# Kernel optimization log

Hardware: AMD Instinct MI355X
Metric: run time of the kernel (lower is better)

## Reference

```python
import jax, jax.numpy as jnp
import numpy as np

NUM_HEADS = 16
NUM_KV_HEADS = 8
HEAD_DIM = 256
HIDDEN = 2048
ROT_DIM = 64          # head_dim * partial_rotary_factor (0.25)
RMS_EPS = 1e-6
ROPE_THETA = 10000.0
SEQ = 2048


def _rmsnorm(x, weight=None):
    # Gemma RMSNorm: x * rsqrt(mean(x^2)+eps) * (1 + w); v_norm has no scale.
    var = jnp.mean(jnp.square(x), axis=-1, keepdims=True)
    n = x * jax.lax.rsqrt(var + RMS_EPS)
    if weight is not None:
        n = n * (1.0 + weight)
    return n


def _rope(x, positions):
    # Partial neox-style RoPE on the first ROT_DIM dims of each head.
    # x: [S, H, D]
    rot, rest = x[..., :ROT_DIM], x[..., ROT_DIM:]
    half = ROT_DIM // 2
    inv_freq = 1.0 / (ROPE_THETA ** (jnp.arange(0, ROT_DIM, 2, dtype=jnp.float32) / ROT_DIM))
    freqs = positions.astype(jnp.float32)[:, None] * inv_freq  # [S, half]
    cos = jnp.cos(freqs)[:, None, :]  # [S, 1, half]
    sin = jnp.sin(freqs)[:, None, :]
    x1, x2 = rot[..., :half], rot[..., half:]
    rot_out = jnp.concatenate([x1 * cos - x2 * sin, x2 * cos + x1 * sin], axis=-1)
    return jnp.concatenate([rot_out, rest], axis=-1)


def setup_inputs() -> dict:
    key = jax.random.key(0)
    k1, k2, k3, k4, k5 = jax.random.split(key, 5)
    q_size = NUM_HEADS * HEAD_DIM
    kv_size = NUM_KV_HEADS * HEAD_DIM
    return {
        "positions": jnp.arange(SEQ, dtype=jnp.int32),
        "hidden_states": jax.random.normal(k1, (SEQ, HIDDEN), dtype=jnp.float32),
        "w_qkv": jax.random.normal(k2, (q_size + 2 * kv_size, HIDDEN), dtype=jnp.float32) * (HIDDEN ** -0.5),
        "q_norm_w": jax.random.normal(k3, (HEAD_DIM,), dtype=jnp.float32) * 0.02,
        "k_norm_w": jax.random.normal(k4, (HEAD_DIM,), dtype=jnp.float32) * 0.02,
        "w_o": jax.random.normal(k5, (HIDDEN, q_size), dtype=jnp.float32) * (q_size ** -0.5),
    }


def reference(positions, hidden_states, w_qkv, q_norm_w, k_norm_w, w_o):
    S = hidden_states.shape[0]
    q_size = NUM_HEADS * HEAD_DIM
    kv_size = NUM_KV_HEADS * HEAD_DIM

    qkv = hidden_states @ w_qkv.T  # [S, q+2kv]
    q, k, v = jnp.split(qkv, [q_size, q_size + kv_size], axis=-1)
    q = q.reshape(S, NUM_HEADS, HEAD_DIM)
    k = k.reshape(S, NUM_KV_HEADS, HEAD_DIM)
    v = v.reshape(S, NUM_KV_HEADS, HEAD_DIM)

    # per-head RMSNorms (v_norm: scale_shift=0, with_scale=False -> pure norm)
    q = _rmsnorm(q, q_norm_w)
    k = _rmsnorm(k, k_norm_w)
    v = _rmsnorm(v, None)

    q = _rope(q, positions)
    k = _rope(k, positions)

    # GQA: repeat kv heads to match query heads
    rep = NUM_HEADS // NUM_KV_HEADS
    k = jnp.repeat(k, rep, axis=1)  # [S, H, D]
    v = jnp.repeat(v, rep, axis=1)

    # RadixAttention constructed with scaling=1.0 -> no 1/sqrt(d) scale
    scores = jnp.einsum("qhd,khd->hqk", q, k)  # [H, S, S]
    causal = positions[:, None] >= positions[None, :]  # [S, S]
    scores = jnp.where(causal[None, :, :], scores, jnp.float32(-1e30))
    attn = jax.nn.softmax(scores, axis=-1)
    out = jnp.einsum("hqk,khd->qhd", attn, v)  # [S, H, D]
    out = out.reshape(S, q_size)
    return out @ w_o.T  # [S, HIDDEN]
```

## Files before the change

### kernel.cpp

```cpp
#include <hip/hip_runtime.h>
#include <stdint.h>
#include <math.h>

#define SEQ 2048
#define HID 2048
#define NH 16
#define NKV 8
#define HD 256
#define QSZ 4096
#define QKVN 8192

typedef __attribute__((ext_vector_type(4))) float f32x4;
typedef _Float16 f16x8 __attribute__((ext_vector_type(8)));
typedef unsigned short u16;

__device__ __forceinline__ u16 f2h(float f) {
  _Float16 h = (_Float16)f;
  return __builtin_bit_cast(u16, h);
}
__device__ __forceinline__ float h2f(u16 b) {
  return (float)__builtin_bit_cast(_Float16, b);
}
__device__ __forceinline__ void glds16(const void* g, void* l) {
  __builtin_amdgcn_global_load_lds(
      (const __attribute__((address_space(1))) uint32_t*)g,
      (__attribute__((address_space(3))) uint32_t*)l, 16, 0, 0);
}

__global__ void cvt_f32_f16(const float* __restrict__ in, u16* __restrict__ out, int n4) {
  int i = blockIdx.x * 256 + threadIdx.x;
  if (i < n4) {
    float4 v = reinterpret_cast<const float4*>(in)[i];
    ushort4 o = make_ushort4(f2h(v.x), f2h(v.y), f2h(v.z), f2h(v.w));
    reinterpret_cast<ushort4*>(out)[i] = o;
  }
}

template <int F16OUT>
__global__ __launch_bounds__(256, 2) void gemm_bt(
    const u16* __restrict__ A, const u16* __restrict__ B, void* __restrict__ Cv,
    int M, int N, int K) {
  __shared__ __align__(16) u16 As[128 * 32];
  __shared__ __align__(16) u16 Bs[128 * 32];
  const int t = threadIdx.x;
  const int w = t >> 6, l = t & 63;
  const int bm = blockIdx.y * 128, bn = blockIdx.x * 128;
  const int wr = (w >> 1) * 64, wc = (w & 1) * 64;
  f32x4 acc[4][4] = {};

  const int arow = t >> 2;
  const int acol = (t & 3) * 8;
  const u16* Ag0 = A + (size_t)(bm + arow) * K + acol;
  const u16* Ag1 = A + (size_t)(bm + 64 + arow) * K + acol;
  const u16* Bg0 = B + (size_t)(bn + arow) * K + acol;
  const u16* Bg1 = B + (size_t)(bn + 64 + arow) * K + acol;
  u16* Al0 = As + w * 512;
  u16* Al1 = As + 2048 + w * 512;
  u16* Bl0 = Bs + w * 512;
  u16* Bl1 = Bs + 2048 + w * 512;

  const int lr = l & 15;
  const int lko = (l >> 4) * 8;

  for (int k0 = 0; k0 < K; k0 += 32) {
    __syncthreads();
    glds16(Ag0 + k0, Al0);
    glds16(Ag1 + k0, Al1);
    glds16(Bg0 + k0, Bl0);
    glds16(Bg1 + k0, Bl1);
    __syncthreads();
    f16x8 a[4], b[4];
#pragma unroll
    for (int m = 0; m < 4; ++m) a[m] = *(const f16x8*)&As[(wr + m * 16 + lr) * 32 + lko];
#pragma unroll
    for (int n = 0; n < 4; ++n) b[n] = *(const f16x8*)&Bs[(wc + n * 16 + lr) * 32 + lko];
#pragma unroll
    for (int m = 0; m < 4; ++m)
#pragma unroll
      for (int n = 0; n < 4; ++n)
        acc[m][n] = __builtin_amdgcn_mfma_f32_16x16x32_f16(a[m], b[n], acc[m][n], 0, 0, 0);
  }

#pragma unroll
  for (int m = 0; m < 4; ++m) {
#pragma unroll
    for (int n = 0; n < 4; ++n) {
      const int col = bn + wc + n * 16 + lr;
      const int row0 = bm + wr + m * 16 + (l >> 4) * 4;
#pragma unroll
      for (int j = 0; j < 4; ++j) {
        float vv = acc[m][n][j];
        if constexpr (F16OUT)
          ((u16*)Cv)[(size_t)(row0 + j) * N + col] = f2h(vv);
        else
          ((float*)Cv)[(size_t)(row0 + j) * N + col] = vv;
      }
    }
  }
}

__global__ void norm_rope(const u16* __restrict__ qkv, const float* __restrict__ qw,
                          const float* __restrict__ kw, const int* __restrict__ pos,
                          u16* __restrict__ qo, u16* __restrict__ ko, u16* __restrict__ vt) {
  const int b = blockIdx.x;
  const int s = b >> 5;
  const int slot = b & 31;
  const int l = threadIdx.x;
  const u16* row = qkv + (size_t)s * QKVN + slot * HD;
  ushort4 rv = *reinterpret_cast<const ushort4*>(row + l * 4);
  float x0 = h2f(rv.x), x1 = h2f(rv.y), x2 = h2f(rv.z), x3 = h2f(rv.w);
  float ss = x0 * x0 + x1 * x1 + x2 * x2 + x3 * x3;
#pragma unroll
  for (int mk = 32; mk; mk >>= 1) ss += __shfl_xor(ss, mk);
  const float rs = rsqrtf(ss * (1.0f / 256.0f) + 1e-6f);
  float n0, n1, n2, n3;
  if (slot < 16) {
    float4 wv = *reinterpret_cast<const float4*>(qw + l * 4);
    n0 = x0 * rs * (1.f + wv.x); n1 = x1 * rs * (1.f + wv.y);
    n2 = x2 * rs * (1.f + wv.z); n3 = x3 * rs * (1.f + wv.w);
  } else if (slot < 24) {
    float4 wv = *reinterpret_cast<const float4*>(kw + l * 4);
    n0 = x0 * rs * (1.f + wv.x); n1 = x1 * rs * (1.f + wv.y);
    n2 = x2 * rs * (1.f + wv.z); n3 = x3 * rs * (1.f + wv.w);
  } else {
    n0 = x0 * rs; n1 = x1 * rs; n2 = x2 * rs; n3 = x3 * rs;
  }
  if (slot < 24) {
    float p0 = __shfl_xor(n0, 8), p1 = __shfl_xor(n1, 8);
    float p2 = __shfl_xor(n2, 8), p3 = __shfl_xor(n3, 8);
    if (l < 16) {
      const double posd = (double)pos[s];
      float v[4] = {n0, n1, n2, n3};
      const float par[4] = {p0, p1, p2, p3};
#pragma unroll
      for (int i = 0; i < 4; ++i) {
        const int d = l * 4 + i;
        const int fi = d & 31;
        double inv = exp2(-(double)fi * (13.287712379549449 / 32.0));
        double ph = posd * inv;
        double tr = ph * 0.15915494309189535;
        tr -= floor(tr);
        float ang = (float)(tr * 6.283185307179586);
        float sn, cs;
        sincosf(ang, &sn, &cs);
        v[i] = (d < 32) ? (v[i] * cs - par[i] * sn) : (v[i] * cs + par[i] * sn);
      }
      n0 = v[0]; n1 = v[1]; n2 = v[2]; n3 = v[3];
    }
  }
  if (slot < 16) {
    ushort4 o = make_ushort4(f2h(n0), f2h(n1), f2h(n2), f2h(n3));
    *reinterpret_cast<ushort4*>(qo + ((size_t)slot * SEQ + s) * HD + l * 4) = o;
  } else if (slot < 24) {
    ushort4 o = make_ushort4(f2h(n0), f2h(n1), f2h(n2), f2h(n3));
    *reinterpret_cast<ushort4*>(ko + ((size_t)(slot - 16) * SEQ + s) * HD + l * 4) = o;
  } else {
    u16* base = vt + (size_t)(slot - 24) * HD * SEQ + s;
    base[(size_t)(l * 4 + 0) * SEQ] = f2h(n0);
    base[(size_t)(l * 4 + 1) * SEQ] = f2h(n1);
    base[(size_t)(l * 4 + 2) * SEQ] = f2h(n2);
    base[(size_t)(l * 4 + 3) * SEQ] = f2h(n3);
  }
}

__global__ __launch_bounds__(512, 1) void attn_fwd(
    const u16* __restrict__ Q, const u16* __restrict__ Kb,
    const u16* __restrict__ Vt, u16* __restrict__ O) {
  __shared__ __align__(16) u16 Ks[2][64 * 256];
  __shared__ __align__(16) u16 Vs[2][256 * 64];
  __shared__ __align__(16) u16 Ps[8 * 16 * 72];
  const int t = threadIdx.x, w = t >> 6, l = t & 63;
  const int bq = (gridDim.x - 1) - blockIdx.x;
  const int h = blockIdx.y;
  const int hk = h >> 1;
  const int lr = l & 15, lg = l >> 4;

  const u16* qrow = Q + ((size_t)h * SEQ + bq * 128 + w * 16 + lr) * HD + lg * 8;
  f16x8 qf[8];
#pragma unroll
  for (int c = 0; c < 8; ++c) qf[c] = *(const f16x8*)(qrow + c * 32);

  float m[4], lsum[4];
#pragma unroll
  for (int j = 0; j < 4; ++j) { m[j] = -1e30f; lsum[j] = 0.f; }
  f32x4 oacc[16] = {};

  const u16* Kg = Kb + (size_t)hk * SEQ * HD;
  const u16* Vg = Vt + (size_t)hk * HD * SEQ;

  auto STAGE = [&](int tt, int buf) {
    const int kv0 = tt * 64;
#pragma unroll
    for (int i = 0; i < 4; ++i) {
      const int seg = i * 8 + w;
      const int r = 2 * seg + (l >> 5);
      const int c = (l & 31) ^ (r & 7);
      glds16(Kg + (size_t)(kv0 + r) * HD + c * 8, &Ks[buf][seg * 512]);
    }
#pragma unroll
    for (int i = 0; i < 4; ++i) {
      const int seg = i * 8 + w;
      const int d = seg * 8 + (l >> 3);
      const int c = (l & 7) ^ (d & 7);
      glds16(Vg + (size_t)d * SEQ + kv0 + c * 8, &Vs[buf][seg * 512]);
    }
  };

  const int nt = (bq + 1) * 2;
  STAGE(0, 0);
  int cur = 0;

  for (int tt = 0; tt < nt; ++tt) {
    if (tt + 1 < nt) {
      STAGE(tt + 1, cur ^ 1);
      asm volatile("s_waitcnt vmcnt(8)" ::: "memory");
    } else {
      asm volatile("s_waitcnt vmcnt(0)" ::: "memory");
    }
    __builtin_amdgcn_s_barrier();

    const int kv0 = tt * 64;
    const u16* Kc = &Ks[cur][0];
    const u16* Vc = &Vs[cur][0];

    f32x4 sv[4];
    __builtin_amdgcn_s_setprio(1);
#pragma unroll
    for (int n = 0; n < 4; ++n) {
      f32x4 s = {};
      const int krow = n * 16 + lr;
      const int rb = krow * 256;
      const int sw = krow & 7;
#pragma unroll
      for (int c = 0; c < 8; ++c) {
        const int chunk = (c * 4 + lg) ^ sw;
        f16x8 kf = *(const f16x8*)&Kc[rb + chunk * 8];
        s = __builtin_amdgcn_mfma_f32_16x16x32_f16(qf[c], kf, s, 0, 0, 0);
      }
      sv[n] = s;
    }
    __builtin_amdgcn_s_setprio(0);
    const int qrow0 = bq * 128 + w * 16 + lg * 4;
    if (kv0 + 63 > bq * 128 + w * 16) {
#pragma unroll
      for (int n = 0; n < 4; ++n) {
        const int col = kv0 + n * 16 + lr;
#pragma unroll
        for (int j = 0; j < 4; ++j)
          if (col > qrow0 + j) sv[n][j] = -1e30f;
      }
    }
    float pvv[4][4];
#pragma unroll
    for (int j = 0; j < 4; ++j) {
      float mx = fmaxf(fmaxf(sv[0][j], sv[1][j]), fmaxf(sv[2][j], sv[3][j]));
#pragma unroll
      for (int mk = 8; mk; mk >>= 1) mx = fmaxf(mx, __shfl_xor(mx, mk));
      if (mx > m[j] + 8.f) {
        const float scale = __expf(m[j] - mx);
        m[j] = mx;
        lsum[j] *= scale;
#pragma unroll
        for (int nc = 0; nc < 16; ++nc) oacc[nc][j] *= scale;
      }
      float rsum = 0.f;
#pragma unroll
      for (int n = 0; n < 4; ++n) {
        float e = __expf(sv[n][j] - m[j]);
        pvv[n][j] = e;
        rsum += e;
      }
#pragma unroll
      for (int mk = 8; mk; mk >>= 1) rsum += __shfl_xor(rsum, mk);
      lsum[j] += rsum;
    }
    u16* pb = Ps + w * 1152;
#pragma unroll
    for (int n = 0; n < 4; ++n)
#pragma unroll
      for (int j = 0; j < 4; ++j)
        pb[(lg * 4 + j) * 72 + n * 16 + lr] = f2h(pvv[n][j]);
    __builtin_amdgcn_s_setprio(1);
#pragma unroll
    for (int kk = 0; kk < 2; ++kk) {
      f16x8 pa = *(const f16x8*)&pb[lr * 72 + kk * 32 + lg * 8];
#pragma unroll
      for (int nc = 0; nc < 16; ++nc) {
        const int drow = nc * 16 + lr;
        const int chunk = (kk * 4 + lg) ^ (drow & 7);
        f16x8 vf = *(const f16x8*)&Vc[drow * 64 + chunk * 8];
        oacc[nc] = __builtin_amdgcn_mfma_f32_16x16x32_f16(pa, vf, oacc[nc], 0, 0, 0);
      }
    }
    __builtin_amdgcn_s_setprio(0);
    __builtin_amdgcn_s_barrier();
    cur ^= 1;
  }
  float rl[4];
#pragma unroll
  for (int j = 0; j < 4; ++j) rl[j] = __fdividef(1.f, lsum[j]);
#pragma unroll
  for (int nc = 0; nc < 16; ++nc) {
#pragma unroll
    for (int j = 0; j < 4; ++j) {
      const int qr = bq * 128 + w * 16 + lg * 4 + j;
      O[(size_t)qr * QSZ + h * HD + nc * 16 + lr] = f2h(oacc[nc][j] * rl[j]);
    }
  }
}

extern "C" void kernel_launch(void* const* d_in, const int* in_sizes, int n_in,
                              void* d_out, int out_size, void* d_ws, size_t ws_size,
                              hipStream_t stream) {
  const int* pos = (const int*)d_in[0];
  const float* hidden = (const float*)d_in[1];
  const float* wqkv = (const float*)d_in[2];
  const float* qw = (const float*)d_in[3];
  const float* kw = (const float*)d_in[4];
  const float* wo_f = (const float*)d_in[5];
  float* out = (float*)d_out;

  char* wsp = (char*)d_ws;
  u16* hb = (u16*)(wsp);
  u16* wqb = (u16*)(wsp + (8ll << 20));
  u16* wob = (u16*)(wsp + (40ll << 20));
  u16* qkvb = (u16*)(wsp + (56ll << 20));
  u16* qb = (u16*)(wsp);
  u16* kb = (u16*)(wsp + (16ll << 20));
  u16* vt = (u16*)(wsp + (24ll << 20));
  u16* ao = (u16*)(wsp + (56ll << 20));

  cvt_f32_f16<<<(HID * HID / 4 + 255) / 256, 256, 0, stream>>>(hidden, hb, HID * HID / 4);
  cvt_f32_f16<<<(QKVN * HID / 4 + 255) / 256, 256, 0, stream>>>(wqkv, wqb, QKVN * HID / 4);
  cvt_f32_f16<<<(HID * QSZ / 4 + 255) / 256, 256, 0, stream>>>(wo_f, wob, HID * QSZ / 4);

  gemm_bt<1><<<dim3(QKVN / 128, SEQ / 128), 256, 0, stream>>>(hb, wqb, (void*)qkvb, SEQ, QKVN, HID);
  norm_rope<<<SEQ * 32, 64, 0, stream>>>(qkvb, qw, kw, pos, qb, kb, vt);
  attn_fwd<<<dim3(SEQ / 128, NH), 512, 0, stream>>>(qb, kb, vt, ao);
  gemm_bt<0><<<dim3(HID / 128, SEQ / 128), 256, 0, stream>>>(ao, wob, (void*)out, SEQ, HID, QSZ);
}
```

Baseline: 362.9 us.

## Give each attention wave two 16-row query tiles and halve waves per block

The attention kernel now runs 4 waves per block instead of 8, and each wave handles 32 query rows (two 16-row MFMA tiles) instead of 16. Each K and V fragment read from LDS feeds two MFMAs, halving LDS read traffic per unit of compute. Each wave now issues twice the staging loads and the wait count is adjusted to match. The cost is roughly double the accumulator and Q registers per wave and fewer waves to hide latency, with a risk of register pressure or spills.

```diff
diff --git a/kernel.cpp b/kernel.cpp
--- a/kernel.cpp
+++ b/kernel.cpp
@@ -163,27 +163,33 @@
   }
 }
 
-__global__ __launch_bounds__(512, 1) void attn_fwd(
+__global__ __launch_bounds__(256, 1) void attn_fwd(
     const u16* __restrict__ Q, const u16* __restrict__ Kb,
     const u16* __restrict__ Vt, u16* __restrict__ O) {
   __shared__ __align__(16) u16 Ks[2][64 * 256];
   __shared__ __align__(16) u16 Vs[2][256 * 64];
-  __shared__ __align__(16) u16 Ps[8 * 16 * 72];
+  __shared__ __align__(16) u16 Ps[4 * 32 * 72];
   const int t = threadIdx.x, w = t >> 6, l = t & 63;
   const int bq = (gridDim.x - 1) - blockIdx.x;
   const int h = blockIdx.y;
   const int hk = h >> 1;
   const int lr = l & 15, lg = l >> 4;
 
-  const u16* qrow = Q + ((size_t)h * SEQ + bq * 128 + w * 16 + lr) * HD + lg * 8;
-  f16x8 qf[8];
-#pragma unroll
-  for (int c = 0; c < 8; ++c) qf[c] = *(const f16x8*)(qrow + c * 32);
-
-  float m[4], lsum[4];
-#pragma unroll
-  for (int j = 0; j < 4; ++j) { m[j] = -1e30f; lsum[j] = 0.f; }
-  f32x4 oacc[16] = {};
+  f16x8 qf[2][8];
+#pragma unroll
+  for (int mi = 0; mi < 2; ++mi) {
+    const u16* qrow =
+        Q + ((size_t)h * SEQ + bq * 128 + w * 32 + mi * 16 + lr) * HD + lg * 8;
+#pragma unroll
+    for (int c = 0; c < 8; ++c) qf[mi][c] = *(const f16x8*)(qrow + c * 32);
+  }
+
+  float m[2][4], lsum[2][4];
+#pragma unroll
+  for (int mi = 0; mi < 2; ++mi)
+#pragma unroll
+    for (int j = 0; j < 4; ++j) { m[mi][j] = -1e30f; lsum[mi][j] = 0.f; }
+  f32x4 oacc[2][16] = {};
 
   const u16* Kg = Kb + (size_t)hk * SEQ * HD;
   const u16* Vg = Vt + (size_t)hk * HD * SEQ;
@@ -191,15 +197,15 @@
   auto STAGE = [&](int tt, int buf) {
     const int kv0 = tt * 64;
 #pragma unroll
-    for (int i = 0; i < 4; ++i) {
-      const int seg = i * 8 + w;
+    for (int i = 0; i < 8; ++i) {
+      const int seg = i * 4 + w;
       const int r = 2 * seg + (l >> 5);
       const int c = (l & 31) ^ (r & 7);
       glds16(Kg + (size_t)(kv0 + r) * HD + c * 8, &Ks[buf][seg * 512]);
     }
 #pragma unroll
-    for (int i = 0; i < 4; ++i) {
-      const int seg = i * 8 + w;
+    for (int i = 0; i < 8; ++i) {
+      const int seg = i * 4 + w;
       const int d = seg * 8 + (l >> 3);
       const int c = (l & 7) ^ (d & 7);
       glds16(Vg + (size_t)d * SEQ + kv0 + c * 8, &Vs[buf][seg * 512]);
@@ -213,7 +219,7 @@
   for (int tt = 0; tt < nt; ++tt) {
     if (tt + 1 < nt) {
       STAGE(tt + 1, cur ^ 1);
-      asm volatile("s_waitcnt vmcnt(8)" ::: "memory");
+      asm volatile("s_waitcnt vmcnt(16)" ::: "memory");
     } else {
       asm volatile("s_waitcnt vmcnt(0)" ::: "memory");
     }
@@ -223,11 +229,11 @@
     const u16* Kc = &Ks[cur][0];
     const u16* Vc = &Vs[cur][0];
 
-    f32x4 sv[4];
+    f32x4 sv[2][4];
     __builtin_amdgcn_s_setprio(1);
 #pragma unroll
     for (int n = 0; n < 4; ++n) {
-      f32x4 s = {};
+      f32x4 s0 = {}, s1 = {};
       const int krow = n * 16 + lr;
       const int rb = krow * 256;
       const int sw = krow & 7;
@@ -235,76 +241,93 @@
       for (int c = 0; c < 8; ++c) {
         const int chunk = (c * 4 + lg) ^ sw;
         f16x8 kf = *(const f16x8*)&Kc[rb + chunk * 8];
-        s = __builtin_amdgcn_mfma_f32_16x16x32_f16(qf[c], kf, s, 0, 0, 0);
-      }
-      sv[n] = s;
+        s0 = __builtin_amdgcn_mfma_f32_16x16x32_f16(qf[0][c], kf, s0, 0, 0, 0);
+        s1 = __builtin_amdgcn_mfma_f32_16x16x32_f16(qf[1][c], kf, s1, 0, 0, 0);
+      }
+      sv[0][n] = s0;
+      sv[1][n] = s1;
     }
     __builtin_amdgcn_s_setprio(0);
-    const int qrow0 = bq * 128 + w * 16 + lg * 4;
-    if (kv0 + 63 > bq * 128 + w * 16) {
-#pragma unroll
-      for (int n = 0; n < 4; ++n) {
-        const int col = kv0 + n * 16 + lr;
+#pragma unroll
+    for (int mi = 0; mi < 2; ++mi) {
+      const int row0 = bq * 128 + w * 32 + mi * 16;
+      if (kv0 + 63 > row0) {
+        const int qrow0 = row0 + lg * 4;
+#pragma unroll
+        for (int n = 0; n < 4; ++n) {
+          const int col = kv0 + n * 16 + lr;
+#pragma unroll
+          for (int j = 0; j < 4; ++j)
+            if (col > qrow0 + j) sv[mi][n][j] = -1e30f;
+        }
+      }
+    }
+    float pvv[2][4][4];
+#pragma unroll
+    for (int mi = 0; mi < 2; ++mi) {
+#pragma unroll
+      for (int j = 0; j < 4; ++j) {
+        float mx = fmaxf(fmaxf(sv[mi][0][j], sv[mi][1][j]),
+                         fmaxf(sv[mi][2][j], sv[mi][3][j]));
+#pragma unroll
+        for (int mk = 8; mk; mk >>= 1) mx = fmaxf(mx, __shfl_xor(mx, mk));
+        if (mx > m[mi][j] + 8.f) {
+          const float scale = __expf(m[mi][j] - mx);
+          m[mi][j] = mx;
+          lsum[mi][j] *= scale;
+#pragma unroll
+          for (int nc = 0; nc < 16; ++nc) oacc[mi][nc][j] *= scale;
+        }
+        float rsum = 0.f;
+#pragma unroll
+        for (int n = 0; n < 4; ++n) {
+          float e = __expf(sv[mi][n][j] - m[mi][j]);
+          pvv[mi][n][j] = e;
+          rsum += e;
+        }
+#pragma unroll
+        for (int mk = 8; mk; mk >>= 1) rsum += __shfl_xor(rsum, mk);
+        lsum[mi][j] += rsum;
+      }
+    }
+    u16* pb = Ps + w * 2304;
+#pragma unroll
+    for (int mi = 0; mi < 2; ++mi)
+#pragma unroll
+      for (int n = 0; n < 4; ++n)
 #pragma unroll
         for (int j = 0; j < 4; ++j)
-          if (col > qrow0 + j) sv[n][j] = -1e30f;
-      }
-    }
-    float pvv[4][4];
-#pragma unroll
-    for (int j = 0; j < 4; ++j) {
-      float mx = fmaxf(fmaxf(sv[0][j], sv[1][j]), fmaxf(sv[2][j], sv[3][j]));
-#pragma unroll
-      for (int mk = 8; mk; mk >>= 1) mx = fmaxf(mx, __shfl_xor(mx, mk));
-      if (mx > m[j] + 8.f) {
-        const float scale = __expf(m[j] - mx);
-        m[j] = mx;
-        lsum[j] *= scale;
-#pragma unroll
-        for (int nc = 0; nc < 16; ++nc) oacc[nc][j] *= scale;
-      }
-      float rsum = 0.f;
-#pragma unroll
-      for (int n = 0; n < 4; ++n) {
-        float e = __expf(sv[n][j] - m[j]);
-        pvv[n][j] = e;
-        rsum += e;
-      }
-#pragma unroll
-      for (int mk = 8; mk; mk >>= 1) rsum += __shfl_xor(rsum, mk);
-      lsum[j] += rsum;
-    }
-    u16* pb = Ps + w * 1152;
-#pragma unroll
-    for (int n = 0; n < 4; ++n)
-#pragma unroll
-      for (int j = 0; j < 4; ++j)
-        pb[(lg * 4 + j) * 72 + n * 16 + lr] = f2h(pvv[n][j]);
+          pb[(mi * 16 + lg * 4 + j) * 72 + n * 16 + lr] = f2h(pvv[mi][n][j]);
     __builtin_amdgcn_s_setprio(1);
 #pragma unroll
     for (int kk = 0; kk < 2; ++kk) {
-      f16x8 pa = *(const f16x8*)&pb[lr * 72 + kk * 32 + lg * 8];
+      f16x8 pa0 = *(const f16x8*)&pb[(lr)*72 + kk * 32 + lg * 8];
+      f16x8 pa1 = *(const f16x8*)&pb[(16 + lr) * 72 + kk * 32 + lg * 8];
 #pragma unroll
       for (int nc = 0; nc < 16; ++nc) {
         const int drow = nc * 16 + lr;
         const int chunk = (kk * 4 + lg) ^ (drow & 7);
         f16x8 vf = *(const f16x8*)&Vc[drow * 64 + chunk * 8];
-        oacc[nc] = __builtin_amdgcn_mfma_f32_16x16x32_f16(pa, vf, oacc[nc], 0, 0, 0);
+        oacc[0][nc] = __builtin_amdgcn_mfma_f32_16x16x32_f16(pa0, vf, oacc[0][nc], 0, 0, 0);
+        oacc[1][nc] = __builtin_amdgcn_mfma_f32_16x16x32_f16(pa1, vf, oacc[1][nc], 0, 0, 0);
       }
     }
     __builtin_amdgcn_s_setprio(0);
     __builtin_amdgcn_s_barrier();
     cur ^= 1;
   }
-  float rl[4];
-#pragma unroll
-  for (int j = 0; j < 4; ++j) rl[j] = __fdividef(1.f, lsum[j]);
-#pragma unroll
-  for (int nc = 0; nc < 16; ++nc) {
-#pragma unroll
-    for (int j = 0; j < 4; ++j) {
-      const int qr = bq * 128 + w * 16 + lg * 4 + j;
-      O[(size_t)qr * QSZ + h * HD + nc * 16 + lr] = f2h(oacc[nc][j] * rl[j]);
+#pragma unroll
+  for (int mi = 0; mi < 2; ++mi) {
+    float rl[4];
+#pragma unroll
+    for (int j = 0; j < 4; ++j) rl[j] = __fdividef(1.f, lsum[mi][j]);
+#pragma unroll
+    for (int nc = 0; nc < 16; ++nc) {
+#pragma unroll
+      for (int j = 0; j < 4; ++j) {
+        const int qr = bq * 128 + w * 32 + mi * 16 + lg * 4 + j;
+        O[(size_t)qr * QSZ + h * HD + nc * 16 + lr] = f2h(oacc[mi][nc][j] * rl[j]);
+      }
     }
   }
 }
@@ -336,6 +359,6 @@
 
   gemm_bt<1><<<dim3(QKVN / 128, SEQ / 128), 256, 0, stream>>>(hb, wqb, (void*)qkvb, SEQ, QKVN, HID);
   norm_rope<<<SEQ * 32, 64, 0, stream>>>(qkvb, qw, kw, pos, qb, kb, vt);
-  attn_fwd<<<dim3(SEQ / 128, NH), 512, 0, stream>>>(qb, kb, vt, ao);
+  attn_fwd<<<dim3(SEQ / 128, NH), 256, 0, stream>>>(qb, kb, vt, ao);
   gemm_bt<0><<<dim3(HID / 128, SEQ / 128), 256, 0, stream>>>(ao, wob, (void*)out, SEQ, HID, QSZ);
 }
```

Result: slower. 444.1 us (+22.4%).

## Split attention KV loop across two wave groups with 64-row query tiles

Applied to the files above, without the earlier changes.

The attention kernel now uses 64-row query blocks, doubling the grid. Each block's 8 waves form two groups that handle alternating 32-wide KV tiles, and the two partial softmax states are merged through shared memory at the end. Launch bounds are raised to allow more blocks per CU, shared memory is shrunk, and the block order is flipped for half the heads to balance causal work. The trade-off is that double-buffered prefetch is dropped in favour of a full vmcnt(0) wait every iteration, and a final merge step is added.

```diff
diff --git a/kernel.cpp b/kernel.cpp
--- a/kernel.cpp
+++ b/kernel.cpp
@@ -163,19 +163,25 @@
   }
 }
 
-__global__ __launch_bounds__(512, 1) void attn_fwd(
+__global__ __launch_bounds__(512, 4) void attn_fwd(
     const u16* __restrict__ Q, const u16* __restrict__ Kb,
     const u16* __restrict__ Vt, u16* __restrict__ O) {
-  __shared__ __align__(16) u16 Ks[2][64 * 256];
-  __shared__ __align__(16) u16 Vs[2][256 * 64];
-  __shared__ __align__(16) u16 Ps[8 * 16 * 72];
+  __shared__ __align__(16) u16 SH[38144];
   const int t = threadIdx.x, w = t >> 6, l = t & 63;
-  const int bq = (gridDim.x - 1) - blockIdx.x;
+  const int g = w >> 2;
+  const int wq = w & 3;
+  const int x = blockIdx.x;
   const int h = blockIdx.y;
+  const int flip = (h >> 3) & 1;
+  const int bq = flip ? x : (31 - x);
   const int hk = h >> 1;
   const int lr = l & 15, lg = l >> 4;
 
-  const u16* qrow = Q + ((size_t)h * SEQ + bq * 128 + w * 16 + lr) * HD + lg * 8;
+  u16* Ksg = SH + g * 8192;
+  u16* Vsg = SH + 16384 + g * 8192;
+  u16* pb = SH + 32768 + w * 640;
+
+  const u16* qrow = Q + ((size_t)h * SEQ + bq * 64 + wq * 16 + lr) * HD + lg * 8;
   f16x8 qf[8];
 #pragma unroll
   for (int c = 0; c < 8; ++c) qf[c] = *(const f16x8*)(qrow + c * 32);
@@ -188,45 +194,32 @@
   const u16* Kg = Kb + (size_t)hk * SEQ * HD;
   const u16* Vg = Vt + (size_t)hk * HD * SEQ;
 
-  auto STAGE = [&](int tt, int buf) {
-    const int kv0 = tt * 64;
+  const int vswz = (lr & 3) ^ ((lr >> 2) & 3);
+
+  for (int it = 0; it <= bq; ++it) {
+    const int kv0 = (2 * it + g) * 32;
 #pragma unroll
     for (int i = 0; i < 4; ++i) {
-      const int seg = i * 8 + w;
+      const int seg = i * 4 + wq;
       const int r = 2 * seg + (l >> 5);
       const int c = (l & 31) ^ (r & 7);
-      glds16(Kg + (size_t)(kv0 + r) * HD + c * 8, &Ks[buf][seg * 512]);
+      glds16(Kg + (size_t)(kv0 + r) * HD + c * 8, Ksg + seg * 512);
     }
 #pragma unroll
     for (int i = 0; i < 4; ++i) {
-      const int seg = i * 8 + w;
-      const int d = seg * 8 + (l >> 3);
-      const int c = (l & 7) ^ (d & 7);
-      glds16(Vg + (size_t)d * SEQ + kv0 + c * 8, &Vs[buf][seg * 512]);
-    }
-  };
-
-  const int nt = (bq + 1) * 2;
-  STAGE(0, 0);
-  int cur = 0;
-
-  for (int tt = 0; tt < nt; ++tt) {
-    if (tt + 1 < nt) {
-      STAGE(tt + 1, cur ^ 1);
-      asm volatile("s_waitcnt vmcnt(8)" ::: "memory");
-    } else {
-      asm volatile("s_waitcnt vmcnt(0)" ::: "memory");
-    }
+      const int seg = i * 4 + wq;
+      const int d = seg * 16 + (l >> 2);
+      const int sz = (d & 3) ^ ((d >> 2) & 3);
+      const int c = (l & 3) ^ sz;
+      glds16(Vg + (size_t)d * SEQ + kv0 + c * 8, Vsg + seg * 512);
+    }
+    asm volatile("s_waitcnt vmcnt(0)" ::: "memory");
     __builtin_amdgcn_s_barrier();
 
-    const int kv0 = tt * 64;
-    const u16* Kc = &Ks[cur][0];
-    const u16* Vc = &Vs[cur][0];
-
-    f32x4 sv[4];
+    f32x4 sv[2];
     __builtin_amdgcn_s_setprio(1);
 #pragma unroll
-    for (int n = 0; n < 4; ++n) {
+    for (int n = 0; n < 2; ++n) {
       f32x4 s = {};
       const int krow = n * 16 + lr;
       const int rb = krow * 256;
@@ -234,26 +227,27 @@
 #pragma unroll
       for (int c = 0; c < 8; ++c) {
         const int chunk = (c * 4 + lg) ^ sw;
-        f16x8 kf = *(const f16x8*)&Kc[rb + chunk * 8];
+        f16x8 kf = *(const f16x8*)&Ksg[rb + chunk * 8];
         s = __builtin_amdgcn_mfma_f32_16x16x32_f16(qf[c], kf, s, 0, 0, 0);
       }
       sv[n] = s;
     }
     __builtin_amdgcn_s_setprio(0);
-    const int qrow0 = bq * 128 + w * 16 + lg * 4;
-    if (kv0 + 63 > bq * 128 + w * 16) {
-#pragma unroll
-      for (int n = 0; n < 4; ++n) {
+    const int row0 = bq * 64 + wq * 16;
+    if (kv0 + 31 > row0) {
+      const int qrow0 = row0 + lg * 4;
+#pragma unroll
+      for (int n = 0; n < 2; ++n) {
         const int col = kv0 + n * 16 + lr;
 #pragma unroll
         for (int j = 0; j < 4; ++j)
           if (col > qrow0 + j) sv[n][j] = -1e30f;
       }
     }
-    float pvv[4][4];
+    float pvv[2][4];
 #pragma unroll
     for (int j = 0; j < 4; ++j) {
-      float mx = fmaxf(fmaxf(sv[0][j], sv[1][j]), fmaxf(sv[2][j], sv[3][j]));
+      float mx = fmaxf(sv[0][j], sv[1][j]);
 #pragma unroll
       for (int mk = 8; mk; mk >>= 1) mx = fmaxf(mx, __shfl_xor(mx, mk));
       if (mx > m[j] + 8.f) {
@@ -265,7 +259,7 @@
       }
       float rsum = 0.f;
 #pragma unroll
-      for (int n = 0; n < 4; ++n) {
+      for (int n = 0; n < 2; ++n) {
         float e = __expf(sv[n][j] - m[j]);
         pvv[n][j] = e;
         rsum += e;
@@ -274,37 +268,58 @@
       for (int mk = 8; mk; mk >>= 1) rsum += __shfl_xor(rsum, mk);
       lsum[j] += rsum;
     }
-    u16* pb = Ps + w * 1152;
-#pragma unroll
-    for (int n = 0; n < 4; ++n)
+#pragma unroll
+    for (int n = 0; n < 2; ++n)
 #pragma unroll
       for (int j = 0; j < 4; ++j)
-        pb[(lg * 4 + j) * 72 + n * 16 + lr] = f2h(pvv[n][j]);
+        pb[(lg * 4 + j) * 40 + n * 16 + lr] = f2h(pvv[n][j]);
+    f16x8 pa = *(const f16x8*)&pb[lr * 40 + lg * 8];
     __builtin_amdgcn_s_setprio(1);
 #pragma unroll
-    for (int kk = 0; kk < 2; ++kk) {
-      f16x8 pa = *(const f16x8*)&pb[lr * 72 + kk * 32 + lg * 8];
-#pragma unroll
-      for (int nc = 0; nc < 16; ++nc) {
-        const int drow = nc * 16 + lr;
-        const int chunk = (kk * 4 + lg) ^ (drow & 7);
-        f16x8 vf = *(const f16x8*)&Vc[drow * 64 + chunk * 8];
-        oacc[nc] = __builtin_amdgcn_mfma_f32_16x16x32_f16(pa, vf, oacc[nc], 0, 0, 0);
-      }
+    for (int nc = 0; nc < 16; ++nc) {
+      const int drow = nc * 16 + lr;
+      const int chunk = lg ^ vswz;
+      f16x8 vf = *(const f16x8*)&Vsg[drow * 32 + chunk * 8];
+      oacc[nc] = __builtin_amdgcn_mfma_f32_16x16x32_f16(pa, vf, oacc[nc], 0, 0, 0);
     }
     __builtin_amdgcn_s_setprio(0);
     __builtin_amdgcn_s_barrier();
-    cur ^= 1;
-  }
-  float rl[4];
-#pragma unroll
-  for (int j = 0; j < 4; ++j) rl[j] = __fdividef(1.f, lsum[j]);
-#pragma unroll
-  for (int nc = 0; nc < 16; ++nc) {
+  }
+
+  if (g == 1) {
+    float* OB = (float*)SH;
+    float* ml = (float*)(SH + 37888);
+#pragma unroll
+    for (int nc = 0; nc < 16; ++nc)
+#pragma unroll
+      for (int j = 0; j < 4; ++j)
+        OB[(wq * 16 + lg * 4 + j) * 256 + nc * 16 + lr] = oacc[nc][j];
+    if (lr == 0) {
+#pragma unroll
+      for (int j = 0; j < 4; ++j) {
+        const int row = wq * 16 + lg * 4 + j;
+        ml[row * 2] = m[j];
+        ml[row * 2 + 1] = lsum[j];
+      }
+    }
+  }
+  __syncthreads();
+  if (g == 0) {
+    const float* OB = (const float*)SH;
+    const float* ml = (const float*)(SH + 37888);
 #pragma unroll
     for (int j = 0; j < 4; ++j) {
-      const int qr = bq * 128 + w * 16 + lg * 4 + j;
-      O[(size_t)qr * QSZ + h * HD + nc * 16 + lr] = f2h(oacc[nc][j] * rl[j]);
+      const int row = wq * 16 + lg * 4 + j;
+      const float mB = ml[row * 2], lB = ml[row * 2 + 1];
+      const float mN = fmaxf(m[j], mB);
+      const float sA = __expf(m[j] - mN), sB = __expf(mB - mN);
+      const float rl = __fdividef(1.f, lsum[j] * sA + lB * sB);
+      const int qr = bq * 64 + row;
+#pragma unroll
+      for (int nc = 0; nc < 16; ++nc) {
+        const float o = (oacc[nc][j] * sA + OB[row * 256 + nc * 16 + lr] * sB) * rl;
+        O[(size_t)qr * QSZ + h * HD + nc * 16 + lr] = f2h(o);
+      }
     }
   }
 }
@@ -336,6 +351,6 @@
 
   gemm_bt<1><<<dim3(QKVN / 128, SEQ / 128), 256, 0, stream>>>(hb, wqb, (void*)qkvb, SEQ, QKVN, HID);
   norm_rope<<<SEQ * 32, 64, 0, stream>>>(qkvb, qw, kw, pos, qb, kb, vt);
-  attn_fwd<<<dim3(SEQ / 128, NH), 512, 0, stream>>>(qb, kb, vt, ao);
+  attn_fwd<<<dim3(SEQ / 64, NH), 512, 0, stream>>>(qb, kb, vt, ao);
   gemm_bt<0><<<dim3(HID / 128, SEQ / 128), 256, 0, stream>>>(ao, wob, (void*)out, SEQ, HID, QSZ);
 }
```

Result: slower. 500.8 us (+38.0%).
